# Kernel tuning notes

Hardware: AMD Instinct MI355X
Metric: run time of the kernel (lower is better)

The kernel has to match this reference:

```python
import jax, jax.numpy as jnp
import numpy as np


def _band_matrix(T, kernel, k):
    """Equivalent of att_I(T): [T,T] banded matrix, row i has k placed on
    columns [i - kernel//2, i + kernel//2] (clipped to [0, T))."""
    kh = kernel // 2
    rows = jnp.arange(T)[:, None]
    cols = jnp.arange(T)[None, :]
    idx = cols - rows + kh  # index into k when in [0, kernel)
    valid = (idx >= 0) & (idx < kernel)
    return jnp.where(valid, k[jnp.clip(idx, 0, kernel - 1)], 0.0)


def setup_inputs() -> dict:
    key = jax.random.key(0)
    k1, k2, k3, k4 = jax.random.split(key, 4)
    N, C, T, V = 16, 64, 512, 25
    kernel, stride = 9, 2
    x = jax.random.normal(k1, (N, C, T, V), dtype=jnp.float32)
    W = jax.random.normal(k2, (C, C), dtype=jnp.float32) * (1.414 / np.sqrt(C))
    alpha = jax.random.normal(k3, (C, C // 4), dtype=jnp.float32) * 0.1
    phi = jax.random.normal(k4, (C, C // 4), dtype=jnp.float32) * 0.1
    k = jnp.ones((kernel,), dtype=jnp.float32) / kernel
    return {"x": x, "W": W, "alpha": alpha, "phi": phi, "k": k,
            "kernel": kernel, "stride": stride}


def reference(x, W, alpha, phi, k, kernel, stride):
    N, C, T, V = x.shape
    d = C // 4
    # [N,V,T,C] projected features
    xp = jnp.einsum('nctv,cd->nvtd', x, W)
    # low-rank Q/K projections
    q = xp @ alpha                     # [N,V,T,d]
    kk = xp @ phi                      # [N,V,T,d]
    att = jnp.einsum('nvtd,nvsd->nvts', q, kk) / d  # [N,V,T,T]
    # dropout is identity in eval mode
    # att_W selects rows 0, stride, 2*stride, ... -> strided slice
    att_ds = att[:, :, ::stride, :]    # [N,V,T',T], T' = ceil(T/stride)
    att_sm = jax.nn.softmax(att_ds, axis=-1)
    I = _band_matrix(T, kernel, k)     # [T,T]
    attention = att_sm + I[::stride, :]  # broadcast [T',T]
    out = jnp.einsum('nvst,nvtd->nvsd', attention, xp)  # [N,V,T',C]
    return out.transpose(0, 3, 2, 1)   # [N,C,T',V]
```

## Files before the change

kernel.cpp:

```cpp
#include <hip/hip_runtime.h>
#include <cstddef>

#define N_  16
#define C_  64
#define T_  512
#define V_  25
#define S_  256
#define M_  (T_ * V_)
#define RS_ (V_ * C_)

typedef short s16x4 __attribute__((ext_vector_type(4)));
typedef float f32x4 __attribute__((ext_vector_type(4)));

__device__ __forceinline__ f32x4 mfma16(s16x4 a, s16x4 b, f32x4 c) {
#if __has_builtin(__builtin_amdgcn_mfma_f32_16x16x16_bf16)
    return __builtin_amdgcn_mfma_f32_16x16x16_bf16(a, b, c, 0, 0, 0);
#elif __has_builtin(__builtin_amdgcn_mfma_f32_16x16x16bf16_1k)
    return __builtin_amdgcn_mfma_f32_16x16x16bf16_1k(a, b, c, 0, 0, 0);
#else
    asm volatile("v_mfma_f32_16x16x16_bf16 %0, %1, %2, %0" : "+v"(c) : "v"(a), "v"(b));
    return c;
#endif
}

__device__ __forceinline__ unsigned packhl(float f) {
    unsigned fb = __float_as_uint(f);
    float hf = __uint_as_float(fb & 0xffff0000u);
    unsigned lb = __float_as_uint(f - hf);
    return (fb >> 16) | (lb & 0xffff0000u);
}
__device__ __forceinline__ unsigned short bhi(float f) {
    return (unsigned short)(__float_as_uint(f) >> 16);
}
__device__ __forceinline__ unsigned short blo(float f) {
    unsigned fb = __float_as_uint(f);
    float hf = __uint_as_float(fb & 0xffff0000u);
    return (unsigned short)(__float_as_uint(f - hf) >> 16);
}
__device__ __forceinline__ s16x4 hi4(uint4 q) {
    return s16x4{(short)(q.x & 0xffffu), (short)(q.y & 0xffffu),
                 (short)(q.z & 0xffffu), (short)(q.w & 0xffffu)};
}
__device__ __forceinline__ s16x4 lo4(uint4 q) {
    return s16x4{(short)(q.x >> 16), (short)(q.y >> 16),
                 (short)(q.z >> 16), (short)(q.w >> 16)};
}
__device__ __forceinline__ s16x4 mk_hi(float a, float b, float c, float d) {
    return s16x4{(short)bhi(a), (short)bhi(b), (short)bhi(c), (short)bhi(d)};
}
__device__ __forceinline__ s16x4 mk_lo(float a, float b, float c, float d) {
    return s16x4{(short)blo(a), (short)blo(b), (short)blo(c), (short)blo(d)};
}

__global__ __launch_bounds__(256, 4) void xp_gemm_kernel(
    const float* __restrict__ x, const float* __restrict__ W,
    float* __restrict__ xp)
{
    const int tid = threadIdx.x, lane = tid & 63, wid = tid >> 6;
    const int l15 = lane & 15, oct = lane >> 4;
    const int n = blockIdx.y;
    const int m0 = blockIdx.x * 256 + wid * 64;
    const float* xb = x + (size_t)n * C_ * M_;

    f32x4 acc[4][4];
    #pragma unroll
    for (int mt = 0; mt < 4; ++mt)
        #pragma unroll
        for (int dt = 0; dt < 4; ++dt) acc[mt][dt] = f32x4{0.f, 0.f, 0.f, 0.f};

    #pragma unroll
    for (int kc = 0; kc < 4; ++kc) {
        const int c0 = kc * 16 + oct * 4;
        s16x4 bh[4], bl[4];
        #pragma unroll
        for (int dt = 0; dt < 4; ++dt) {
            const float* wb = W + (size_t)c0 * C_ + dt * 16 + l15;
            float w0 = wb[0], w1 = wb[C_], w2 = wb[2 * C_], w3 = wb[3 * C_];
            bh[dt] = mk_hi(w0, w1, w2, w3);
            bl[dt] = mk_lo(w0, w1, w2, w3);
        }
        #pragma unroll
        for (int mt = 0; mt < 4; ++mt) {
            const float* xc = xb + (size_t)c0 * M_ + m0 + mt * 16 + l15;
            float x0 = xc[0], x1 = xc[M_], x2 = xc[2 * (size_t)M_], x3 = xc[3 * (size_t)M_];
            s16x4 ah = mk_hi(x0, x1, x2, x3);
            s16x4 al = mk_lo(x0, x1, x2, x3);
            #pragma unroll
            for (int dt = 0; dt < 4; ++dt) {
                acc[mt][dt] = mfma16(ah, bh[dt], acc[mt][dt]);
                acc[mt][dt] = mfma16(ah, bl[dt], acc[mt][dt]);
                acc[mt][dt] = mfma16(al, bh[dt], acc[mt][dt]);
            }
        }
    }
    float* ob = xp + ((size_t)n * M_ + m0) * C_;
    #pragma unroll
    for (int mt = 0; mt < 4; ++mt)
        #pragma unroll
        for (int dt = 0; dt < 4; ++dt)
            #pragma unroll
            for (int r = 0; r < 4; ++r)
                ob[(size_t)(mt * 16 + oct * 4 + r) * C_ + dt * 16 + l15] = acc[mt][dt][r];
}

__global__ __launch_bounds__(512, 4) void attn_kernel(
    const float* __restrict__ xp, const float* __restrict__ alpha,
    const float* __restrict__ phi, float* __restrict__ tmp)
{
    __shared__ unsigned smem[16192];
    unsigned* Pu  = smem;
    unsigned* Qu  = smem + 9216;
    unsigned* Xu  = smem + 9216;
    unsigned* KKu = smem + 9216 + 4608;
    float* phiT = (float*)(smem + 15104);
    float* alT  = (float*)smem;

    const int tid = threadIdx.x;
    const int lane = tid & 63;
    const int wid = tid >> 6;
    const int l15 = lane & 15;
    const int oct = lane >> 4;
    const int nv = blockIdx.x;
    const int n = nv / V_, v = nv - n * V_;
    const float* xpb = xp + (size_t)n * M_ * C_ + (size_t)v * C_;

    for (int i = tid; i < 1024; i += 512) {
        int c = i >> 4, e = i & 15;
        alT[e * 68 + c]  = alpha[i] * 0.0625f;
        phiT[e * 68 + c] = phi[i];
    }
    __syncthreads();

    {
        int s = tid >> 1, eh = tid & 1;
        const float* xr = xpb + (size_t)(2 * s) * RS_;
        const float* ab = alT + (eh * 8) * 68;
        float qa[8] = {0.f, 0.f, 0.f, 0.f, 0.f, 0.f, 0.f, 0.f};
        #pragma unroll
        for (int c4 = 0; c4 < 16; ++c4) {
            float4 xv = *(const float4*)(xr + c4 * 4);
            #pragma unroll
            for (int j = 0; j < 8; ++j) {
                float4 av = *(const float4*)(ab + j * 68 + c4 * 4);
                qa[j] += xv.x * av.x + xv.y * av.y + xv.z * av.z + xv.w * av.w;
            }
        }
        unsigned* qp = Qu + s * 20 + eh * 8;
        *(uint4*)(qp)     = uint4{packhl(qa[0]), packhl(qa[1]), packhl(qa[2]), packhl(qa[3])};
        *(uint4*)(qp + 4) = uint4{packhl(qa[4]), packhl(qa[5]), packhl(qa[6]), packhl(qa[7])};
    }
    __syncthreads();

    const int s0w = wid * 32;
    s16x4 qh[2], ql[2];
    #pragma unroll
    for (int st = 0; st < 2; ++st) {
        uint4 qv = *(const uint4*)(Qu + (size_t)(s0w + st * 16 + l15) * 20 + oct * 4);
        qh[st] = hi4(qv); ql[st] = lo4(qv);
    }
    __syncthreads();

    auto STAGE = [&](int ch, int buf) {
        int t = tid >> 4, d4 = tid & 15;
        float4 xv = *(const float4*)(xpb + (size_t)(ch * 32 + t) * RS_ + d4 * 4);
        unsigned short* Xh = (unsigned short*)(Xu + buf * 2304);
        unsigned short* Xl = (unsigned short*)(Xu + buf * 2304 + 1152);
        float vals[4] = {xv.x, xv.y, xv.z, xv.w};
        #pragma unroll
        for (int i = 0; i < 4; ++i) {
            int d = d4 * 4 + i;
            int tp = t ^ ((d & 7) << 2);
            Xh[d * 36 + tp] = bhi(vals[i]);
            Xl[d * 36 + tp] = blo(vals[i]);
        }
    };
    auto KKDOTS = [&](int ch, int buf) {
        int t = tid & 31, e = tid >> 5;
        const float* xr = xpb + (size_t)(ch * 32 + t) * RS_;
        const float* pb = phiT + e * 68;
        float a = 0.f;
        #pragma unroll
        for (int c4 = 0; c4 < 16; ++c4) {
            float4 xv = *(const float4*)(xr + c4 * 4);
            float4 pv = *(const float4*)(pb + c4 * 4);
            a += xv.x * pv.x + xv.y * pv.y + xv.z * pv.z + xv.w * pv.w;
        }
        KKu[buf * 640 + t * 20 + e] = packhl(a);
    };

    STAGE(0, 0); KKDOTS(0, 0);
    __syncthreads();

    f32x4 acc[2][4];
    #pragma unroll
    for (int st = 0; st < 2; ++st)
        #pragma unroll
        for (int dt = 0; dt < 4; ++dt) acc[st][dt] = f32x4{0.f, 0.f, 0.f, 0.f};
    float lp[2] = {0.f, 0.f};
    unsigned* Pw = Pu + wid * 1152;

    for (int c = 0; c < 16; ++c) {
        const int cur = c & 1;
        if (c < 15) { STAGE(c + 1, cur ^ 1); KKDOTS(c + 1, cur ^ 1); }

        s16x4 kh[2], kl[2];
        #pragma unroll
        for (int tt = 0; tt < 2; ++tt) {
            uint4 kf = *(const uint4*)(KKu + cur * 640 + (tt * 16 + l15) * 20 + oct * 4);
            kh[tt] = hi4(kf); kl[tt] = lo4(kf);
        }
        #pragma unroll
        for (int st = 0; st < 2; ++st) {
            #pragma unroll
            for (int tt = 0; tt < 2; ++tt) {
                f32x4 d = {0.f, 0.f, 0.f, 0.f};
                d = mfma16(kh[tt], qh[st], d);
                d = mfma16(kh[tt], ql[st], d);
                d = mfma16(kl[tt], qh[st], d);
                float p0 = __expf(d[0]), p1 = __expf(d[1]);
                float p2 = __expf(d[2]), p3 = __expf(d[3]);
                lp[st] += (p0 + p1) + (p2 + p3);
                *(uint4*)(Pw + (st * 16 + l15) * 36 + tt * 16 + oct * 4) =
                    uint4{packhl(p0), packhl(p1), packhl(p2), packhl(p3)};
            }
        }

        const unsigned* Xh32 = Xu + cur * 2304;
        const unsigned* Xl32 = Xu + cur * 2304 + 1152;
        #pragma unroll
        for (int kt = 0; kt < 2; ++kt) {
            s16x4 pah[2], pal[2];
            #pragma unroll
            for (int st = 0; st < 2; ++st) {
                uint4 pv = *(const uint4*)(Pw + (st * 16 + l15) * 36 + kt * 16 + oct * 4);
                pah[st] = hi4(pv); pal[st] = lo4(pv);
            }
            #pragma unroll
            for (int dt = 0; dt < 4; ++dt) {
                int d = dt * 16 + l15;
                int g4 = (kt * 16 + oct * 4) ^ ((d & 7) << 2);
                int i0 = d * 18 + (g4 >> 1);
                unsigned xa = Xh32[i0], xb2 = Xh32[i0 + 1];
                s16x4 xh = s16x4{(short)(xa & 0xffffu), (short)(xa >> 16),
                                 (short)(xb2 & 0xffffu), (short)(xb2 >> 16)};
                xa = Xl32[i0]; xb2 = Xl32[i0 + 1];
                s16x4 xl = s16x4{(short)(xa & 0xffffu), (short)(xa >> 16),
                                 (short)(xb2 & 0xffffu), (short)(xb2 >> 16)};
                #pragma unroll
                for (int st = 0; st < 2; ++st) {
                    acc[st][dt] = mfma16(pah[st], xh, acc[st][dt]);
                    acc[st][dt] = mfma16(pah[st], xl, acc[st][dt]);
                    acc[st][dt] = mfma16(pal[st], xh, acc[st][dt]);
                }
            }
        }
        __syncthreads();
    }

    #pragma unroll
    for (int st = 0; st < 2; ++st) {
        lp[st] += __shfl_xor(lp[st], 16);
        lp[st] += __shfl_xor(lp[st], 32);
    }
    float* ob = tmp + (size_t)nv * S_ * C_;
    #pragma unroll
    for (int st = 0; st < 2; ++st) {
        float rl[4];
        #pragma unroll
        for (int r = 0; r < 4; ++r)
            rl[r] = 1.0f / __shfl(lp[st], (lane & 48) | (oct * 4 + r));
        #pragma unroll
        for (int dt = 0; dt < 4; ++dt)
            #pragma unroll
            for (int r = 0; r < 4; ++r) {
                int s = s0w + st * 16 + oct * 4 + r;
                ob[(size_t)s * C_ + dt * 16 + l15] = acc[st][dt][r] * rl[r];
            }
    }
}

__global__ __launch_bounds__(256) void final_kernel(
    const float* __restrict__ tmp, const float* __restrict__ xp,
    const float* __restrict__ kband, float* __restrict__ out)
{
    __shared__ float lt[V_ * 8 * 65];
    __shared__ float kbl[9];
    const int tid = threadIdx.x;
    const int b = blockIdx.x;
    const int n = b >> 5, st = b & 31, s0 = st * 8;
    if (tid < 9) kbl[tid] = kband[tid];
    __syncthreads();

    const float* tb = tmp + ((size_t)n * V_ * S_ + s0) * C_;
    const float* xb = xp + (size_t)n * M_ * C_;
    for (int i = tid; i < V_ * 8 * 16; i += 256) {
        int vv = i >> 7, r = i & 127;
        int si = r >> 4, c4 = (r & 15) * 4;
        int s = s0 + si;
        float4 val = *(const float4*)(tb + ((size_t)vv * S_ + si) * C_ + c4);
        #pragma unroll
        for (int j = 0; j < 9; ++j) {
            int t = 2 * s + j - 4;
            if ((unsigned)t < (unsigned)T_) {
                float kb = kbl[j];
                float4 xv = *(const float4*)(xb + ((size_t)t * V_ + vv) * C_ + c4);
                val.x += kb * xv.x; val.y += kb * xv.y;
                val.z += kb * xv.z; val.w += kb * xv.w;
            }
        }
        float* dst = lt + (vv * 8 + si) * 65 + c4;
        dst[0] = val.x; dst[1] = val.y; dst[2] = val.z; dst[3] = val.w;
    }
    __syncthreads();
    float* ob = out + (size_t)n * (C_ * S_ * V_) + (size_t)s0 * V_;
    for (int i = tid; i < C_ * 8 * V_; i += 256) {
        int d = i / 200;
        int r = i - d * 200;
        int si = r / 25;
        int vv = r - si * 25;
        ob[(size_t)d * (S_ * V_) + si * V_ + vv] = lt[(vv * 8 + si) * 65 + d];
    }
}

extern "C" void kernel_launch(void* const* d_in, const int* in_sizes, int n_in,
                              void* d_out, int out_size, void* d_ws, size_t ws_size,
                              hipStream_t stream)
{
    const float* x     = (const float*)d_in[0];
    const float* W     = (const float*)d_in[1];
    const float* alpha = (const float*)d_in[2];
    const float* phi   = (const float*)d_in[3];
    const float* kband = (const float*)d_in[4];

    float* xp  = (float*)d_ws;
    float* tmp = xp + (size_t)N_ * M_ * C_;

    xp_gemm_kernel<<<dim3(M_ / 256, N_), 256, 0, stream>>>(x, W, xp);
    attn_kernel<<<dim3(N_ * V_), 512, 0, stream>>>(xp, alpha, phi, tmp);
    final_kernel<<<dim3(N_ * 32), 256, 0, stream>>>(tmp, xp, kband, (float*)d_out);
}
```

Before: 285.6 us.

## Keep softmax probabilities in registers and repack X tile as packed hi/lo

The attention kernel no longer writes exp-scores to shared memory and reads them back. The QK tile is produced in the lane layout the PV MFMA needs and packed straight into bf16 hi/lo operands (mk_hi/mk_lo). The X chunk is staged as interleaved hi/lo words, so one uint4 LDS read replaces four scalar reads, and shared memory shrinks from about 64KB to 32KB, which could raise occupancy. The final output writer now uses 200 threads that each loop over channels instead of 256 threads doing index division, which lowers write parallelism. Staging X now makes strided scalar global reads per column instead of float4 row reads.

```diff
diff --git a/kernel.cpp b/kernel.cpp
--- a/kernel.cpp
+++ b/kernel.cpp
@@ -107,13 +107,12 @@
     const float* __restrict__ xp, const float* __restrict__ alpha,
     const float* __restrict__ phi, float* __restrict__ tmp)
 {
-    __shared__ unsigned smem[16192];
-    unsigned* Pu  = smem;
-    unsigned* Qu  = smem + 9216;
-    unsigned* Xu  = smem + 9216;
-    unsigned* KKu = smem + 9216 + 4608;
-    float* phiT = (float*)(smem + 15104);
-    float* alT  = (float*)smem;
+    __shared__ unsigned smem[8064];
+    unsigned* Xu  = smem;
+    unsigned* KKu = smem + 4608;
+    float* phiT = (float*)(smem + 5888);
+    float* alT  = (float*)(smem + 6976);
+    unsigned* Qu  = smem;
 
     const int tid = threadIdx.x;
     const int lane = tid & 63;
@@ -161,18 +160,13 @@
     __syncthreads();
 
     auto STAGE = [&](int ch, int buf) {
-        int t = tid >> 4, d4 = tid & 15;
-        float4 xv = *(const float4*)(xpb + (size_t)(ch * 32 + t) * RS_ + d4 * 4);
-        unsigned short* Xh = (unsigned short*)(Xu + buf * 2304);
-        unsigned short* Xl = (unsigned short*)(Xu + buf * 2304 + 1152);
-        float vals[4] = {xv.x, xv.y, xv.z, xv.w};
-        #pragma unroll
-        for (int i = 0; i < 4; ++i) {
-            int d = d4 * 4 + i;
-            int tp = t ^ ((d & 7) << 2);
-            Xh[d * 36 + tp] = bhi(vals[i]);
-            Xl[d * 36 + tp] = blo(vals[i]);
-        }
+        int d = tid & 63, tq = tid >> 6;
+        const float* col = xpb + (size_t)(ch * 32 + tq * 4) * RS_ + d;
+        unsigned u0 = packhl(col[0]);
+        unsigned u1 = packhl(col[RS_]);
+        unsigned u2 = packhl(col[2 * RS_]);
+        unsigned u3 = packhl(col[3 * RS_]);
+        *(uint4*)(Xu + buf * 2304 + d * 36 + tq * 4) = uint4{u0, u1, u2, u3};
     };
     auto KKDOTS = [&](int ch, int buf) {
         int t = tid & 31, e = tid >> 5;
@@ -197,60 +191,39 @@
         #pragma unroll
         for (int dt = 0; dt < 4; ++dt) acc[st][dt] = f32x4{0.f, 0.f, 0.f, 0.f};
     float lp[2] = {0.f, 0.f};
-    unsigned* Pw = Pu + wid * 1152;
 
     for (int c = 0; c < 16; ++c) {
         const int cur = c & 1;
         if (c < 15) { STAGE(c + 1, cur ^ 1); KKDOTS(c + 1, cur ^ 1); }
-
-        s16x4 kh[2], kl[2];
-        #pragma unroll
-        for (int tt = 0; tt < 2; ++tt) {
-            uint4 kf = *(const uint4*)(KKu + cur * 640 + (tt * 16 + l15) * 20 + oct * 4);
-            kh[tt] = hi4(kf); kl[tt] = lo4(kf);
-        }
-        #pragma unroll
-        for (int st = 0; st < 2; ++st) {
-            #pragma unroll
-            for (int tt = 0; tt < 2; ++tt) {
-                f32x4 d = {0.f, 0.f, 0.f, 0.f};
-                d = mfma16(kh[tt], qh[st], d);
-                d = mfma16(kh[tt], ql[st], d);
-                d = mfma16(kl[tt], qh[st], d);
-                float p0 = __expf(d[0]), p1 = __expf(d[1]);
-                float p2 = __expf(d[2]), p3 = __expf(d[3]);
+        const unsigned* Xb = Xu + cur * 2304;
+        const unsigned* Kb = KKu + cur * 640;
+
+        #pragma unroll
+        for (int kt = 0; kt < 2; ++kt) {
+            uint4 kf = *(const uint4*)(Kb + (kt * 16 + l15) * 20 + oct * 4);
+            s16x4 kh = hi4(kf), kl = lo4(kf);
+            s16x4 ph[2], pl[2];
+            #pragma unroll
+            for (int st = 0; st < 2; ++st) {
+                f32x4 dqk = {0.f, 0.f, 0.f, 0.f};
+                dqk = mfma16(kh, qh[st], dqk);
+                dqk = mfma16(kh, ql[st], dqk);
+                dqk = mfma16(kl, qh[st], dqk);
+                float p0 = __expf(dqk[0]), p1 = __expf(dqk[1]);
+                float p2 = __expf(dqk[2]), p3 = __expf(dqk[3]);
                 lp[st] += (p0 + p1) + (p2 + p3);
-                *(uint4*)(Pw + (st * 16 + l15) * 36 + tt * 16 + oct * 4) =
-                    uint4{packhl(p0), packhl(p1), packhl(p2), packhl(p3)};
-            }
-        }
-
-        const unsigned* Xh32 = Xu + cur * 2304;
-        const unsigned* Xl32 = Xu + cur * 2304 + 1152;
-        #pragma unroll
-        for (int kt = 0; kt < 2; ++kt) {
-            s16x4 pah[2], pal[2];
-            #pragma unroll
-            for (int st = 0; st < 2; ++st) {
-                uint4 pv = *(const uint4*)(Pw + (st * 16 + l15) * 36 + kt * 16 + oct * 4);
-                pah[st] = hi4(pv); pal[st] = lo4(pv);
+                ph[st] = mk_hi(p0, p1, p2, p3);
+                pl[st] = mk_lo(p0, p1, p2, p3);
             }
             #pragma unroll
             for (int dt = 0; dt < 4; ++dt) {
-                int d = dt * 16 + l15;
-                int g4 = (kt * 16 + oct * 4) ^ ((d & 7) << 2);
-                int i0 = d * 18 + (g4 >> 1);
-                unsigned xa = Xh32[i0], xb2 = Xh32[i0 + 1];
-                s16x4 xh = s16x4{(short)(xa & 0xffffu), (short)(xa >> 16),
-                                 (short)(xb2 & 0xffffu), (short)(xb2 >> 16)};
-                xa = Xl32[i0]; xb2 = Xl32[i0 + 1];
-                s16x4 xl = s16x4{(short)(xa & 0xffffu), (short)(xa >> 16),
-                                 (short)(xb2 & 0xffffu), (short)(xb2 >> 16)};
+                uint4 xf = *(const uint4*)(Xb + (dt * 16 + l15) * 36 + kt * 16 + oct * 4);
+                s16x4 xh = hi4(xf), xl = lo4(xf);
                 #pragma unroll
                 for (int st = 0; st < 2; ++st) {
-                    acc[st][dt] = mfma16(pah[st], xh, acc[st][dt]);
-                    acc[st][dt] = mfma16(pah[st], xl, acc[st][dt]);
-                    acc[st][dt] = mfma16(pal[st], xh, acc[st][dt]);
+                    acc[st][dt] = mfma16(ph[st], xh, acc[st][dt]);
+                    acc[st][dt] = mfma16(ph[st], xl, acc[st][dt]);
+                    acc[st][dt] = mfma16(pl[st], xh, acc[st][dt]);
                 }
             }
         }
@@ -312,13 +285,13 @@
         dst[0] = val.x; dst[1] = val.y; dst[2] = val.z; dst[3] = val.w;
     }
     __syncthreads();
-    float* ob = out + (size_t)n * (C_ * S_ * V_) + (size_t)s0 * V_;
-    for (int i = tid; i < C_ * 8 * V_; i += 256) {
-        int d = i / 200;
-        int r = i - d * 200;
-        int si = r / 25;
-        int vv = r - si * 25;
-        ob[(size_t)d * (S_ * V_) + si * V_ + vv] = lt[(vv * 8 + si) * 65 + d];
+    if (tid < 200) {
+        int si = tid / 25, vv = tid - si * 25;
+        const float* src = lt + (vv * 8 + si) * 65;
+        float* ob = out + (size_t)n * (C_ * S_ * V_) + (size_t)(s0 + si) * V_ + vv;
+        #pragma unroll 8
+        for (int d = 0; d < C_; ++d)
+            ob[(size_t)d * (S_ * V_)] = src[d];
     }
 }
 
```

Result: no change. 287.8 us (+0.7%).
